# Kernel optimization log

Hardware: AMD Instinct MI355X
Metric: run time of the kernel (lower is better)

Reference implementation:

```python
import jax, jax.numpy as jnp
import numpy as np

FORGET_BIAS = 1.0  # TF LSTMCell default


def _lstm_layer(x_tbd, kernel, bias):
    """x_tbd: [T, B, D]; kernel: [D+H, 4H] (gate order i, j, f, o); returns [T, B, H]."""
    H = kernel.shape[1] // 4
    B = x_tbd.shape[1]
    c0 = jnp.zeros((B, H), dtype=x_tbd.dtype)
    h0 = jnp.zeros((B, H), dtype=x_tbd.dtype)

    def step(carry, x_t):
        c, h = carry
        gates = jnp.concatenate([x_t, h], axis=-1) @ kernel + bias
        i, j, f, o = jnp.split(gates, 4, axis=-1)
        c = jax.nn.sigmoid(f + FORGET_BIAS) * c + jax.nn.sigmoid(i) * jnp.tanh(j)
        h = jax.nn.sigmoid(o) * jnp.tanh(c)
        return (c, h), h

    _, hs = jax.lax.scan(step, (c0, h0), x_tbd)
    return hs


def setup_inputs() -> dict:
    key = jax.random.key(0)
    ks = jax.random.split(key, 4)
    B, T, H, C = 64, 1024, 256, 6
    x = jax.random.normal(ks[0], (B, T, H), dtype=jnp.float32)
    kernel0 = jax.random.normal(ks[1], (2 * H, 4 * H), dtype=jnp.float32) * 0.05
    bias0 = jnp.zeros((4 * H,), dtype=jnp.float32)
    kernel1 = jax.random.normal(ks[2], (2 * H, 4 * H), dtype=jnp.float32) * 0.05
    bias1 = jnp.zeros((4 * H,), dtype=jnp.float32)
    w_out = jax.random.normal(ks[3], (H, C), dtype=jnp.float32)
    b_out = jnp.zeros((C,), dtype=jnp.float32)
    return {"x": x, "kernel0": kernel0, "bias0": bias0,
            "kernel1": kernel1, "bias1": bias1,
            "w_out": w_out, "b_out": b_out}


def reference(x, kernel0, bias0, kernel1, bias1, w_out, b_out):
    # testing=True => keep_prob=1.0 (dropout is identity)
    x_tbd = jnp.transpose(x, (1, 0, 2))        # [T, B, D]
    h1 = _lstm_layer(x_tbd, kernel0, bias0)    # [T, B, H]
    h2 = _lstm_layer(h1, kernel1, bias1)       # [T, B, H]
    # sequence_length == T for every batch row => gather last timestep
    last = h2[-1]                              # [B, H]
    logits = last @ w_out + b_out              # [B, C]
    output = jax.nn.sigmoid(logits)
    prediction = jnp.where(output > 0.5,
                           jnp.ones_like(output), jnp.zeros_like(output))
    return logits, output, prediction
```

## Files before the change

### kernel.cpp

```cpp
#include <hip/hip_runtime.h>
#include <math.h>


#define BB 64
#define TT 1024
#define HH 256
#define NTHREADS 512
#define GRPBLKS 64
#define FLAG_STRIDE 16
#define FLAG_INTS (4 * GRPBLKS * FLAG_STRIDE)
#define FLAG_BYTES ((((size_t)FLAG_INTS * 4) + 255) & ~(size_t)255)
#define HBUF_FLOATS (BB * HH)
#define WT_FLOATS (256 * 4 * 512)
#define WS_NEEDED (FLAG_BYTES + (size_t)4 * HBUF_FLOATS * 4 + (size_t)2 * WT_FLOATS * 4)

#define HROW 576

typedef float f32x4 __attribute__((ext_vector_type(4)));

__device__ __forceinline__ void coh_store(float* p, float v) {
  __hip_atomic_store(p, v, __ATOMIC_RELAXED, __HIP_MEMORY_SCOPE_AGENT);
}

__device__ __forceinline__ void coh_load4(
    const float* p0, const float* p1, const float* p2, const float* p3,
    f32x4& a0, f32x4& a1, f32x4& a2, f32x4& a3) {
  asm volatile(
      "global_load_dwordx4 %0, %4, off sc0 sc1\n\t"
      "global_load_dwordx4 %1, %5, off sc0 sc1\n\t"
      "global_load_dwordx4 %2, %6, off sc0 sc1\n\t"
      "global_load_dwordx4 %3, %7, off sc0 sc1\n\t"
      "s_waitcnt vmcnt(0)"
      : "=&v"(a0), "=&v"(a1), "=&v"(a2), "=&v"(a3)
      : "v"(p0), "v"(p1), "v"(p2), "v"(p3)
      : "memory");
}

__global__ void transpose_w(const float* __restrict__ src, float* __restrict__ dst) {
  __shared__ float t[64][65];
  const int g  = blockIdx.x;
  const int kt = blockIdx.y;
  const int ut = blockIdx.z;
  const int tx = threadIdx.x & 63;
  const int ty = threadIdx.x >> 6;
  #pragma unroll
  for (int r = ty; r < 64; r += 4)
    t[r][tx] = src[(size_t)(kt * 64 + r) * 1024 + g * 256 + ut * 64 + tx];
  __syncthreads();
  #pragma unroll
  for (int r = ty; r < 64; r += 4)
    dst[((size_t)(ut * 64 + r) * 4 + g) * 512 + kt * 64 + tx] = t[tx][r];
}

__global__ __launch_bounds__(NTHREADS, 2) void lstm2_persistent(
    const float* __restrict__ x,
    const float* __restrict__ b0, const float* __restrict__ b1,
    const float* __restrict__ wt0, const float* __restrict__ wt1,
    float* __restrict__ hws, int* __restrict__ flags)
{
  __shared__ float hstage[16 * HROW];
  __shared__ f32x4 part[128 * 17];

  const int blk   = blockIdx.x;
  const int taskB = blk >= 128;
  const int tblk  = taskB ? blk - 128 : blk;
  const int bgrp  = tblk >> 5;
  const int ublk  = tblk & 31;

  const int tid = threadIdx.x;
  const int ul  = tid & 7;
  const int kq  = (tid >> 3) & 15;
  const int bt  = tid >> 7;
  const int c   = tid & 127;
  const int r0  = tid >> 7;

  const float* WT   = taskB ? wt1 : wt0;
  const float* bias = taskB ? b1 : b0;

  f32x4 w[4][8];
  {
    const float* wb = WT + (size_t)(ublk * 8 + ul) * 2048 + kq * 32;
    #pragma unroll
    for (int g = 0; g < 4; ++g)
      #pragma unroll
      for (int cc = 0; cc < 8; ++cc)
        w[g][cc] = *(const f32x4*)(wb + g * 512 + cc * 4);
  }

  float bi = 0.f, bj = 0.f, bfv = 0.f, bo = 0.f;
  if (tid < 128) {
    const int u = ublk * 8 + (tid & 7);
    bi  = bias[u];
    bj  = bias[256 + u];
    bfv = bias[512 + u];
    bo  = bias[768 + u];
  }
  float cst = 0.f;

  float* h1b0 = hws;
  float* h1b1 = hws + HBUF_FLOATS;
  float* h2b0 = hws + 2 * HBUF_FLOATS;
  float* h2b1 = hws + 3 * HBUF_FLOATS;

  const int dpos = c * 4 + (c >> 3) * 4;

  for (int s = 0; s <= TT; ++s) {
    const bool active = taskB ? (s >= 1) : (s < TT);
    if (active) {
      const int t = taskB ? (s - 1) : s;
      const float* h1prev = ((s - 1) & 1) ? h1b1 : h1b0;

      f32x4 v0, v1, v2, v3;
      if (!taskB && c < 64) {
        const float* bx = x + (size_t)t * HH + c * 4;
        v0 = *(const f32x4*)(bx + (size_t)(bgrp * 16 + r0 + 0)  * ((size_t)TT * HH));
        v1 = *(const f32x4*)(bx + (size_t)(bgrp * 16 + r0 + 4)  * ((size_t)TT * HH));
        v2 = *(const f32x4*)(bx + (size_t)(bgrp * 16 + r0 + 8)  * ((size_t)TT * HH));
        v3 = *(const f32x4*)(bx + (size_t)(bgrp * 16 + r0 + 12) * ((size_t)TT * HH));
      } else {
        const float* src;
        int kk;
        if (!taskB)      { src = h1prev; kk = (c - 64) * 4; }
        else if (c < 64) { src = h1prev; kk = c * 4; }
        else {
          const float* h2prev = (s & 1) ? h2b1 : h2b0;
          src = h2prev; kk = (c - 64) * 4;
        }
        const float* p0 = src + (size_t)(bgrp * 16 + r0) * HH + kk;
        coh_load4(p0, p0 + 4 * HH, p0 + 8 * HH, p0 + 12 * HH, v0, v1, v2, v3);
      }
      *(f32x4*)&hstage[(r0 + 0)  * HROW + dpos] = v0;
      *(f32x4*)&hstage[(r0 + 4)  * HROW + dpos] = v1;
      *(f32x4*)&hstage[(r0 + 8)  * HROW + dpos] = v2;
      *(f32x4*)&hstage[(r0 + 12) * HROW + dpos] = v3;
      __syncthreads();

      float acc[4][4];
      #pragma unroll
      for (int b4 = 0; b4 < 4; ++b4)
        #pragma unroll
        for (int g = 0; g < 4; ++g) acc[b4][g] = 0.f;

      const int kbase = kq * 36;
      #pragma unroll
      for (int b4 = 0; b4 < 4; ++b4) {
        const float* hp = &hstage[(bt * 4 + b4) * HROW + kbase];
        #pragma unroll
        for (int cc = 0; cc < 8; ++cc) {
          const f32x4 h4 = *(const f32x4*)(hp + cc * 4);
          #pragma unroll
          for (int g = 0; g < 4; ++g) {
            acc[b4][g] = fmaf(h4[0], w[g][cc][0], acc[b4][g]);
            acc[b4][g] = fmaf(h4[1], w[g][cc][1], acc[b4][g]);
            acc[b4][g] = fmaf(h4[2], w[g][cc][2], acc[b4][g]);
            acc[b4][g] = fmaf(h4[3], w[g][cc][3], acc[b4][g]);
          }
        }
      }

      #pragma unroll
      for (int b4 = 0; b4 < 4; ++b4) {
        f32x4 p = { acc[b4][0], acc[b4][1], acc[b4][2], acc[b4][3] };
        part[((bt * 4 + b4) * 8 + ul) * 17 + kq] = p;
      }
      __syncthreads();

      if (tid < 128) {
        float gi = bi, gj = bj, gf = bfv, go = bo;
        #pragma unroll
        for (int q = 0; q < 16; ++q) {
          const f32x4 p = part[tid * 17 + q];
          gi += p[0]; gj += p[1]; gf += p[2]; go += p[3];
        }
        const float ig = 1.f / (1.f + expf(-gi));
        const float jt = tanhf(gj);
        const float fg = 1.f / (1.f + expf(-(gf + 1.0f)));
        const float og = 1.f / (1.f + expf(-go));
        cst = fg * cst + ig * jt;
        const float hn = og * tanhf(cst);
        float* hbout;
        if (!taskB) hbout = (s & 1) ? h1b1 : h1b0;
        else        hbout = ((s - 1) & 1) ? h2b1 : h2b0;
        coh_store(hbout + (size_t)(bgrp * 16 + (tid >> 3)) * HH + ublk * 8 + (tid & 7), hn);
      }
    }

    if (s < TT) {
      __syncthreads();
      if (tid == 0) {
        __hip_atomic_store(&flags[(bgrp * GRPBLKS + (taskB ? 32 : 0) + ublk) * FLAG_STRIDE],
                           s + 1, __ATOMIC_RELAXED, __HIP_MEMORY_SCOPE_AGENT);
      }
      if (tid < GRPBLKS) {
        const int* fp = &flags[(bgrp * GRPBLKS + tid) * FLAG_STRIDE];
        for (;;) {
          const int v = __hip_atomic_load(fp, __ATOMIC_RELAXED, __HIP_MEMORY_SCOPE_AGENT);
          if (__all(v > s)) break;
          __builtin_amdgcn_s_sleep(2);
        }
      }
      __syncthreads();
    }
  }
}

__global__ void head_kernel(const float* __restrict__ h2last,
                            const float* __restrict__ w_out,
                            const float* __restrict__ b_out,
                            float* __restrict__ out)
{
  int tid = threadIdx.x;
  if (tid >= 384) return;
  int bb = tid / 6, cc = tid % 6;
  float acc = b_out[cc];
  const float* hr = h2last + bb * HH;
  #pragma unroll 4
  for (int uu = 0; uu < HH; ++uu) acc = fmaf(hr[uu], w_out[uu * 6 + cc], acc);
  out[tid] = acc;
  float sg = 1.f / (1.f + expf(-acc));
  out[384 + tid] = sg;
  out[768 + tid] = (sg > 0.5f) ? 1.f : 0.f;
}

extern "C" void kernel_launch(void* const* d_in, const int* in_sizes, int n_in,
                              void* d_out, int out_size, void* d_ws, size_t ws_size,
                              hipStream_t stream) {
  const float* x     = (const float*)d_in[0];
  const float* k0    = (const float*)d_in[1];
  const float* b0    = (const float*)d_in[2];
  const float* k1    = (const float*)d_in[3];
  const float* b1    = (const float*)d_in[4];
  const float* w_out = (const float*)d_in[5];
  const float* b_out = (const float*)d_in[6];
  float* out = (float*)d_out;

  if (ws_size < WS_NEEDED) return;

  int*   flags = (int*)d_ws;
  float* hws   = (float*)((char*)d_ws + FLAG_BYTES);
  float* wt0   = hws + 4 * HBUF_FLOATS;
  float* wt1   = wt0 + WT_FLOATS;

  hipMemsetAsync(d_ws, 0, FLAG_BYTES + (size_t)4 * HBUF_FLOATS * 4, stream);

  transpose_w<<<dim3(4, 8, 4), 256, 0, stream>>>(k0, wt0);
  transpose_w<<<dim3(4, 8, 4), 256, 0, stream>>>(k1, wt1);

  lstm2_persistent<<<256, NTHREADS, 0, stream>>>(x, b0, b1, wt0, wt1, hws, flags);

  head_kernel<<<1, 384, 0, stream>>>(hws + 3 * HBUF_FLOATS, w_out, b_out, out);
}
```

Baseline: 3.969 ms.

## Replace lockstep global barrier with per-wave dependency flags and 4-deep h ring buffers

Removes the per-step all-block barrier in favor of fine-grained dataflow waits. Each wave polls only the producer flags it needs (layer-0 h for layer 1, the previous own-layer h, and a lag-3 check for ring reuse). Blocks write per-wave flags after their h stores, and h buffers become 4-slot rings, so layer 0 and layer 1 can drift apart instead of running in lockstep. The change also drops the s=0..TT skew loop and remaps thread roles so the input-load waves line up with the dependency they wait on. Correctness now depends on the memory-ordering subtleties of the relaxed flag and store protocol.

```diff
diff --git a/kernel.cpp b/kernel.cpp
--- a/kernel.cpp
+++ b/kernel.cpp
@@ -6,19 +6,21 @@
 #define TT 1024
 #define HH 256
 #define NTHREADS 512
-#define GRPBLKS 64
-#define FLAG_STRIDE 16
-#define FLAG_INTS (4 * GRPBLKS * FLAG_STRIDE)
-#define FLAG_BYTES ((((size_t)FLAG_INTS * 4) + 255) & ~(size_t)255)
+#define FLAG_BYTES 4096
 #define HBUF_FLOATS (BB * HH)
+#define HSET_FLOATS (4 * HBUF_FLOATS)
 #define WT_FLOATS (256 * 4 * 512)
-#define WS_NEEDED (FLAG_BYTES + (size_t)4 * HBUF_FLOATS * 4 + (size_t)2 * WT_FLOATS * 4)
-
+#define WS_NEEDED (FLAG_BYTES + (size_t)2 * HSET_FLOATS * 4 + (size_t)2 * WT_FLOATS * 4)
 #define HROW 576
+#define NEG_INF_THR (-1000000)
 
 typedef float f32x4 __attribute__((ext_vector_type(4)));
+typedef int   i32x2 __attribute__((ext_vector_type(2)));
 
 __device__ __forceinline__ void coh_store(float* p, float v) {
+  __hip_atomic_store(p, v, __ATOMIC_RELAXED, __HIP_MEMORY_SCOPE_AGENT);
+}
+__device__ __forceinline__ void coh_store_i(int* p, int v) {
   __hip_atomic_store(p, v, __ATOMIC_RELAXED, __HIP_MEMORY_SCOPE_AGENT);
 }
 
@@ -34,6 +36,19 @@
       : "=&v"(a0), "=&v"(a1), "=&v"(a2), "=&v"(a3)
       : "v"(p0), "v"(p1), "v"(p2), "v"(p3)
       : "memory");
+}
+
+__device__ __forceinline__ void poll_wave(const int* fp, int thr) {
+  for (;;) {
+    i32x2 f;
+    asm volatile(
+        "global_load_dwordx2 %0, %1, off sc0 sc1\n\t"
+        "s_waitcnt vmcnt(0)"
+        : "=v"(f) : "v"(fp) : "memory");
+    const int v = f[0] < f[1] ? f[0] : f[1];
+    if (__all(v >= thr)) break;
+    __builtin_amdgcn_s_sleep(1);
+  }
 }
 
 __global__ void transpose_w(const float* __restrict__ src, float* __restrict__ dst) {
@@ -56,7 +71,8 @@
     const float* __restrict__ x,
     const float* __restrict__ b0, const float* __restrict__ b1,
     const float* __restrict__ wt0, const float* __restrict__ wt1,
-    float* __restrict__ hws, int* __restrict__ flags)
+    float* __restrict__ h1buf, float* __restrict__ h2buf,
+    int* __restrict__ flags)
 {
   __shared__ float hstage[16 * HROW];
   __shared__ f32x4 part[128 * 17];
@@ -67,12 +83,16 @@
   const int bgrp  = tblk >> 5;
   const int ublk  = tblk & 31;
 
-  const int tid = threadIdx.x;
-  const int ul  = tid & 7;
-  const int kq  = (tid >> 3) & 15;
-  const int bt  = tid >> 7;
-  const int c   = tid & 127;
-  const int r0  = tid >> 7;
+  const int tid  = threadIdx.x;
+  const int wv   = tid >> 6;
+  const int lane = tid & 63;
+  const int ul   = tid & 7;
+  const int kq   = ((tid >> 8) << 3) | ((tid >> 3) & 7);
+  const int bt   = (tid >> 6) & 3;
+  const bool lowW = (wv < 4);
+  const int cS   = (tid & 63) + (lowW ? 0 : 64);
+  const int rS   = (tid >> 6) & 3;
+  const int dposS = cS * 4 + (cS >> 3) * 4;
 
   const float* WT   = taskB ? wt1 : wt0;
   const float* bias = taskB ? b1 : b0;
@@ -97,109 +117,87 @@
   }
   float cst = 0.f;
 
-  float* h1b0 = hws;
-  float* h1b1 = hws + HBUF_FLOATS;
-  float* h2b0 = hws + 2 * HBUF_FLOATS;
-  float* h2b1 = hws + 3 * HBUF_FLOATS;
-
-  const int dpos = c * 4 + (c >> 3) * 4;
-
-  for (int s = 0; s <= TT; ++s) {
-    const bool active = taskB ? (s >= 1) : (s < TT);
-    if (active) {
-      const int t = taskB ? (s - 1) : s;
-      const float* h1prev = ((s - 1) & 1) ? h1b1 : h1b0;
-
-      f32x4 v0, v1, v2, v3;
-      if (!taskB && c < 64) {
-        const float* bx = x + (size_t)t * HH + c * 4;
-        v0 = *(const f32x4*)(bx + (size_t)(bgrp * 16 + r0 + 0)  * ((size_t)TT * HH));
-        v1 = *(const f32x4*)(bx + (size_t)(bgrp * 16 + r0 + 4)  * ((size_t)TT * HH));
-        v2 = *(const f32x4*)(bx + (size_t)(bgrp * 16 + r0 + 8)  * ((size_t)TT * HH));
-        v3 = *(const f32x4*)(bx + (size_t)(bgrp * 16 + r0 + 12) * ((size_t)TT * HH));
+  const int* pollp  = flags + ((size_t)bgrp * 64 + lane) * 2;
+  int*       myflag = flags + ((size_t)bgrp * 64 + (taskB ? 32 : 0) + ublk) * 2;
+
+  for (int t = 0; t < TT; ++t) {
+    f32x4 v0, v1, v2, v3;
+    if (lowW) {
+      if (!taskB) {
+        const float* bx = x + ((size_t)(bgrp * 16 + rS) * TT + t) * HH + (tid & 63) * 4;
+        const size_t rstep = (size_t)4 * TT * HH;
+        v0 = *(const f32x4*)(bx);
+        v1 = *(const f32x4*)(bx + rstep);
+        v2 = *(const f32x4*)(bx + 2 * rstep);
+        v3 = *(const f32x4*)(bx + 3 * rstep);
       } else {
-        const float* src;
-        int kk;
-        if (!taskB)      { src = h1prev; kk = (c - 64) * 4; }
-        else if (c < 64) { src = h1prev; kk = c * 4; }
-        else {
-          const float* h2prev = (s & 1) ? h2b1 : h2b0;
-          src = h2prev; kk = (c - 64) * 4;
-        }
-        const float* p0 = src + (size_t)(bgrp * 16 + r0) * HH + kk;
+        poll_wave(pollp, (lane < 32) ? (t + 1) : NEG_INF_THR);
+        const float* p0 = h1buf + (size_t)(t & 3) * HBUF_FLOATS
+                        + (size_t)(bgrp * 16 + rS) * HH + (tid & 63) * 4;
         coh_load4(p0, p0 + 4 * HH, p0 + 8 * HH, p0 + 12 * HH, v0, v1, v2, v3);
       }
-      *(f32x4*)&hstage[(r0 + 0)  * HROW + dpos] = v0;
-      *(f32x4*)&hstage[(r0 + 4)  * HROW + dpos] = v1;
-      *(f32x4*)&hstage[(r0 + 8)  * HROW + dpos] = v2;
-      *(f32x4*)&hstage[(r0 + 12) * HROW + dpos] = v3;
-      __syncthreads();
-
-      float acc[4][4];
-      #pragma unroll
-      for (int b4 = 0; b4 < 4; ++b4)
+    } else {
+      const int thr = taskB ? ((lane < 32) ? NEG_INF_THR : t)
+                            : ((lane < 32) ? t : (t - 3));
+      poll_wave(pollp, thr);
+      const float* src = (taskB ? h2buf : h1buf) + (size_t)((t - 1) & 3) * HBUF_FLOATS;
+      const float* p0 = src + (size_t)(bgrp * 16 + rS) * HH + (tid & 63) * 4;
+      coh_load4(p0, p0 + 4 * HH, p0 + 8 * HH, p0 + 12 * HH, v0, v1, v2, v3);
+    }
+    *(f32x4*)&hstage[(rS + 0)  * HROW + dposS] = v0;
+    *(f32x4*)&hstage[(rS + 4)  * HROW + dposS] = v1;
+    *(f32x4*)&hstage[(rS + 8)  * HROW + dposS] = v2;
+    *(f32x4*)&hstage[(rS + 12) * HROW + dposS] = v3;
+    __syncthreads();
+
+    float acc[4][4];
+    #pragma unroll
+    for (int b4 = 0; b4 < 4; ++b4)
+      #pragma unroll
+      for (int g = 0; g < 4; ++g) acc[b4][g] = 0.f;
+
+    const int kbase = kq * 36;
+    #pragma unroll
+    for (int b4 = 0; b4 < 4; ++b4) {
+      const float* hp = &hstage[(bt * 4 + b4) * HROW + kbase];
+      #pragma unroll
+      for (int cc = 0; cc < 8; ++cc) {
+        const f32x4 h4 = *(const f32x4*)(hp + cc * 4);
         #pragma unroll
-        for (int g = 0; g < 4; ++g) acc[b4][g] = 0.f;
-
-      const int kbase = kq * 36;
-      #pragma unroll
-      for (int b4 = 0; b4 < 4; ++b4) {
-        const float* hp = &hstage[(bt * 4 + b4) * HROW + kbase];
-        #pragma unroll
-        for (int cc = 0; cc < 8; ++cc) {
-          const f32x4 h4 = *(const f32x4*)(hp + cc * 4);
-          #pragma unroll
-          for (int g = 0; g < 4; ++g) {
-            acc[b4][g] = fmaf(h4[0], w[g][cc][0], acc[b4][g]);
-            acc[b4][g] = fmaf(h4[1], w[g][cc][1], acc[b4][g]);
-            acc[b4][g] = fmaf(h4[2], w[g][cc][2], acc[b4][g]);
-            acc[b4][g] = fmaf(h4[3], w[g][cc][3], acc[b4][g]);
-          }
+        for (int g = 0; g < 4; ++g) {
+          acc[b4][g] = fmaf(h4[0], w[g][cc][0], acc[b4][g]);
+          acc[b4][g] = fmaf(h4[1], w[g][cc][1], acc[b4][g]);
+          acc[b4][g] = fmaf(h4[2], w[g][cc][2], acc[b4][g]);
+          acc[b4][g] = fmaf(h4[3], w[g][cc][3], acc[b4][g]);
         }
       }
-
-      #pragma unroll
-      for (int b4 = 0; b4 < 4; ++b4) {
-        f32x4 p = { acc[b4][0], acc[b4][1], acc[b4][2], acc[b4][3] };
-        part[((bt * 4 + b4) * 8 + ul) * 17 + kq] = p;
+    }
+
+    #pragma unroll
+    for (int b4 = 0; b4 < 4; ++b4) {
+      f32x4 p = { acc[b4][0], acc[b4][1], acc[b4][2], acc[b4][3] };
+      part[((bt * 4 + b4) * 8 + ul) * 17 + kq] = p;
+    }
+    __syncthreads();
+
+    if (tid < 128) {
+      float gi = bi, gj = bj, gf = bfv, go = bo;
+      #pragma unroll
+      for (int q = 0; q < 16; ++q) {
+        const f32x4 p = part[tid * 17 + q];
+        gi += p[0]; gj += p[1]; gf += p[2]; go += p[3];
       }
-      __syncthreads();
-
-      if (tid < 128) {
-        float gi = bi, gj = bj, gf = bfv, go = bo;
-        #pragma unroll
-        for (int q = 0; q < 16; ++q) {
-          const f32x4 p = part[tid * 17 + q];
-          gi += p[0]; gj += p[1]; gf += p[2]; go += p[3];
-        }
-        const float ig = 1.f / (1.f + expf(-gi));
-        const float jt = tanhf(gj);
-        const float fg = 1.f / (1.f + expf(-(gf + 1.0f)));
-        const float og = 1.f / (1.f + expf(-go));
-        cst = fg * cst + ig * jt;
-        const float hn = og * tanhf(cst);
-        float* hbout;
-        if (!taskB) hbout = (s & 1) ? h1b1 : h1b0;
-        else        hbout = ((s - 1) & 1) ? h2b1 : h2b0;
-        coh_store(hbout + (size_t)(bgrp * 16 + (tid >> 3)) * HH + ublk * 8 + (tid & 7), hn);
-      }
-    }
-
-    if (s < TT) {
-      __syncthreads();
-      if (tid == 0) {
-        __hip_atomic_store(&flags[(bgrp * GRPBLKS + (taskB ? 32 : 0) + ublk) * FLAG_STRIDE],
-                           s + 1, __ATOMIC_RELAXED, __HIP_MEMORY_SCOPE_AGENT);
-      }
-      if (tid < GRPBLKS) {
-        const int* fp = &flags[(bgrp * GRPBLKS + tid) * FLAG_STRIDE];
-        for (;;) {
-          const int v = __hip_atomic_load(fp, __ATOMIC_RELAXED, __HIP_MEMORY_SCOPE_AGENT);
-          if (__all(v > s)) break;
-          __builtin_amdgcn_s_sleep(2);
-        }
-      }
-      __syncthreads();
+      const float ig = 1.f / (1.f + expf(-gi));
+      const float jt = tanhf(gj);
+      const float fg = 1.f / (1.f + expf(-(gf + 1.0f)));
+      const float og = 1.f / (1.f + expf(-go));
+      cst = fg * cst + ig * jt;
+      const float hn = og * tanhf(cst);
+
+      float* hb = (taskB ? h2buf : h1buf) + (size_t)(t & 3) * HBUF_FLOATS;
+      coh_store(hb + (size_t)(bgrp * 16 + (tid >> 3)) * HH + ublk * 8 + (tid & 7), hn);
+      asm volatile("s_waitcnt vmcnt(0)" ::: "memory");
+      if ((tid & 63) == 0) coh_store_i(myflag + (tid >> 6), t + 1);
     }
   }
 }
@@ -237,16 +235,18 @@
   if (ws_size < WS_NEEDED) return;
 
   int*   flags = (int*)d_ws;
-  float* hws   = (float*)((char*)d_ws + FLAG_BYTES);
-  float* wt0   = hws + 4 * HBUF_FLOATS;
+  float* h1b   = (float*)((char*)d_ws + FLAG_BYTES);
+  float* h2b   = h1b + HSET_FLOATS;
+  float* wt0   = h2b + HSET_FLOATS;
   float* wt1   = wt0 + WT_FLOATS;
 
-  hipMemsetAsync(d_ws, 0, FLAG_BYTES + (size_t)4 * HBUF_FLOATS * 4, stream);
+  hipMemsetAsync(d_ws, 0, FLAG_BYTES + (size_t)2 * HSET_FLOATS * 4, stream);
 
   transpose_w<<<dim3(4, 8, 4), 256, 0, stream>>>(k0, wt0);
   transpose_w<<<dim3(4, 8, 4), 256, 0, stream>>>(k1, wt1);
 
-  lstm2_persistent<<<256, NTHREADS, 0, stream>>>(x, b0, b1, wt0, wt1, hws, flags);
-
-  head_kernel<<<1, 384, 0, stream>>>(hws + 3 * HBUF_FLOATS, w_out, b_out, out);
-}
+  lstm2_persistent<<<256, NTHREADS, 0, stream>>>(x, b0, b1, wt0, wt1,
+                                                 h1b, h2b, flags);
+
+  head_kernel<<<1, 384, 0, stream>>>(h2b + 3 * HBUF_FLOATS, w_out, b_out, out);
+}
```

Result: slower. 7.154 ms (+80.2%).
